# Optimization experiments

Measured on AMD Instinct MI355X. Metric: run time of the kernel, lower is better.

The kernel has to match this reference:

```python
import jax, jax.numpy as jnp
import numpy as np

SCALE = 0.08838834764831845  # 1/sqrt(head_size=128)
B, H, D, BS, NB, X, MAX_BLOCKS = 32, 16, 128, 16, 2048, 8, 64
S = MAX_BLOCKS * BS  # max context = 1024


def setup_inputs() -> dict:
    key = jax.random.key(0)
    ks = jax.random.split(key, 6)
    query = jax.random.normal(ks[0], (B, H, D), dtype=jnp.float32)
    new_k = jax.random.normal(ks[1], (B, H, D), dtype=jnp.float32)
    new_v = jax.random.normal(ks[2], (B, H, D), dtype=jnp.float32)
    # vLLM paged layouts: key [NB, H, D//X, BS, X], value [NB, H, BS, D]
    key_cache = jax.random.normal(ks[3], (NB, H, D // X, BS, X), dtype=jnp.float32)
    value_cache = jax.random.normal(ks[4], (NB, H, BS, D), dtype=jnp.float32)
    # non-overlapping block tables: seq i owns blocks [i*64, (i+1)*64)
    block_tables = jnp.arange(B * MAX_BLOCKS, dtype=jnp.int32).reshape(B, MAX_BLOCKS)
    context_lens = jax.random.randint(ks[5], (B,), 256, S + 1).astype(jnp.int32)
    last = context_lens - 1  # slot of the token being decoded
    slot_mapping = (block_tables[jnp.arange(B), last // BS] * BS + last % BS).astype(jnp.int32)
    return dict(query=query, key=new_k, value=new_v, key_cache=key_cache,
                value_cache=value_cache, block_tables=block_tables,
                context_lens=context_lens, slot_mapping=slot_mapping)


def reference(query, key, value, key_cache, value_cache, block_tables, context_lens, slot_mapping):
    nb, h, hsx, bs, x = key_cache.shape
    d = hsx * x
    # flatten paged caches to [nb*bs, h, d] slot-major views
    k_flat = jnp.transpose(key_cache, (0, 3, 1, 2, 4)).reshape(nb * bs, h, d)
    v_flat = jnp.transpose(value_cache, (0, 2, 1, 3)).reshape(nb * bs, h, d)
    # ops.reshape_and_cache: write the new token's k/v into its slot
    k_flat = k_flat.at[slot_mapping].set(key)
    v_flat = v_flat.at[slot_mapping].set(value)
    # single_query_cached_kv_attention, fully vectorized over tokens
    s = block_tables.shape[1] * bs
    pos = jnp.arange(s)
    tok = block_tables[:, pos // bs] * bs + pos % bs        # [B, S] flat slot ids
    keys = k_flat[tok]                                       # [B, S, H, D] gather
    vals = v_flat[tok]                                       # [B, S, H, D]
    scores = jnp.einsum('bhd,bshd->bhs', query, keys) * jnp.float32(SCALE)
    mask = pos[None, :] < context_lens[:, None]              # valid context positions
    scores = jnp.where(mask[:, None, :], scores, jnp.float32(-1e9))
    attn = jax.nn.softmax(scores, axis=-1)
    out = jnp.einsum('bhs,bshd->bhd', attn, vals)            # [B, H, D]
    return out.reshape(out.shape[0], h * d)
```

## Files before the change

### kernel.cpp

```cpp
#include <hip/hip_runtime.h>
#include <math.h>

#define BB 32
#define HH 16
#define DD 128
#define BSZ 16
#define MAXBLK 64
#define NCHUNK 4
#define CT 256
#define CBLK 16
#define SCALE 0.08838834764831845f

__global__ __launch_bounds__(256) void attn_chunk_kernel(
    const float* __restrict__ q, const float* __restrict__ newk,
    const float* __restrict__ newv, const float* __restrict__ kc,
    const float* __restrict__ vc, const int* __restrict__ block_tables,
    const int* __restrict__ context_lens,
    float* __restrict__ o_part, float* __restrict__ m_part,
    float* __restrict__ l_part)
{
    __shared__ __align__(16) float s_scores[CT];
    __shared__ __align__(16) float s_q[DD];
    __shared__ float s_red[8];
    __shared__ __align__(16) float s_out[4][DD];

    int gid  = blockIdx.x;
    int c    = gid & (NCHUNK - 1);
    int bh   = gid >> 2;
    int b    = bh >> 4;
    int h    = bh & 15;
    int tid  = threadIdx.x;
    int wave = tid >> 6;
    int lane = tid & 63;

    int len    = context_lens[b];
    int cstart = c * CT;
    if (cstart >= len) return;

    int nblk   = (len + 15) >> 4;
    int cb0    = c * CBLK;
    int cb_end = min(nblk, cb0 + CBLK);
    int last   = len - 1;
    bool haslast = (last >> 8) == c;

    if (tid < DD) s_q[tid] = q[(size_t)bh * DD + tid] * SCALE;
    __syncthreads();

    int hi = lane >> 5;
    int xq = lane & 1;
    int tk = (lane >> 1) & 15;

    float4 rq[8];
#pragma unroll
    for (int ch = 0; ch < 8; ++ch)
        rq[ch] = *(const float4*)&s_q[(2 * ch + hi) * 8 + 4 * xq];

    const int* bt = block_tables + b * MAXBLK;

    for (int cb = cb0 + wave; cb < cb_end; cb += 4) {
        int pb = bt[cb];
        const float* kbase = kc + ((size_t)pb * HH + h) * 2048 + 4 * lane;
        float acc = 0.f;
#pragma unroll
        for (int ch = 0; ch < 8; ++ch) {
            float4 kv = *(const float4*)(kbase + ch * 256);
            acc += rq[ch].x * kv.x + rq[ch].y * kv.y
                 + rq[ch].z * kv.z + rq[ch].w * kv.w;
        }
        acc += __shfl_xor(acc, 1);
        acc += __shfl_xor(acc, 32);
        if (lane < 32 && (lane & 1) == 0) {
            int p = cb * 16 + tk;
            s_scores[(cb - cb0) * 16 + tk] = (p < len) ? acc : -INFINITY;
        }
    }
    __syncthreads();

    if (haslast && wave == 0) {
        float2 nk = *(const float2*)&newk[(size_t)bh * DD + 2 * lane];
        float part = s_q[2 * lane] * nk.x + s_q[2 * lane + 1] * nk.y;
#pragma unroll
        for (int off = 32; off; off >>= 1) part += __shfl_xor(part, off);
        if (lane == 0) s_scores[last - cstart] = part;
    }
    __syncthreads();

    int padded = (cb_end - cb0) * 16;
    float mloc = (tid < padded) ? s_scores[tid] : -INFINITY;
#pragma unroll
    for (int off = 32; off; off >>= 1) mloc = fmaxf(mloc, __shfl_xor(mloc, off));
    if (lane == 0) s_red[wave] = mloc;
    __syncthreads();
    float m = fmaxf(fmaxf(s_red[0], s_red[1]), fmaxf(s_red[2], s_red[3]));

    float e = 0.f;
    if (tid < padded) {
        e = __expf(s_scores[tid] - m);
        s_scores[tid] = e;
    }
    float ssum = e;
#pragma unroll
    for (int off = 32; off; off >>= 1) ssum += __shfl_xor(ssum, off);
    if (lane == 0) s_red[4 + wave] = ssum;
    __syncthreads();
    float lsum = s_red[4] + s_red[5] + s_red[6] + s_red[7];

    int dv = 4 * (lane & 31);
    float4 nv4 = make_float4(0.f, 0.f, 0.f, 0.f);
    if (haslast) nv4 = *(const float4*)&newv[(size_t)bh * DD + dv];
    int lastTok = haslast ? last : -1;

    float4 acc4 = make_float4(0.f, 0.f, 0.f, 0.f);
    for (int cb = cb0 + wave; cb < cb_end; cb += 4) {
        int pb = bt[cb];
        const float* vbase = vc + ((size_t)pb * HH + h) * 2048 + 4 * lane;
        int base_s = (cb - cb0) * 16 + hi;
        int base_p = cb * 16 + hi;
#pragma unroll
        for (int t2 = 0; t2 < 8; ++t2) {
            float w = s_scores[base_s + 2 * t2];
            float4 vv = *(const float4*)(vbase + t2 * 256);
            if (base_p + 2 * t2 == lastTok) vv = nv4;
            acc4.x += w * vv.x;
            acc4.y += w * vv.y;
            acc4.z += w * vv.z;
            acc4.w += w * vv.w;
        }
    }
    acc4.x += __shfl_xor(acc4.x, 32);
    acc4.y += __shfl_xor(acc4.y, 32);
    acc4.z += __shfl_xor(acc4.z, 32);
    acc4.w += __shfl_xor(acc4.w, 32);
    if (lane < 32) *(float4*)&s_out[wave][dv] = acc4;
    __syncthreads();

    if (tid < DD) {
        float o = s_out[0][tid] + s_out[1][tid] + s_out[2][tid] + s_out[3][tid];
        o_part[(size_t)gid * DD + tid] = o;
    }
    if (tid == 0) {
        m_part[gid] = m;
        l_part[gid] = lsum;
    }
}

__global__ __launch_bounds__(128) void attn_combine_kernel(
    const float* __restrict__ o_part, const float* __restrict__ m_part,
    const float* __restrict__ l_part, const int* __restrict__ context_lens,
    float* __restrict__ out)
{
    int bh  = blockIdx.x;
    int b   = bh >> 4;
    int tid = threadIdx.x;
    int len = context_lens[b];
    int nc  = (len + CT - 1) >> 8;

    float mi[NCHUNK];
    float m_g = -INFINITY;
    for (int i = 0; i < nc; ++i) {
        mi[i] = m_part[bh * NCHUNK + i];
        m_g = fmaxf(m_g, mi[i]);
    }
    float acc = 0.f, lg = 0.f;
    for (int i = 0; i < nc; ++i) {
        float w = __expf(mi[i] - m_g);
        lg  += w * l_part[bh * NCHUNK + i];
        acc += w * o_part[(size_t)(bh * NCHUNK + i) * DD + tid];
    }
    out[(size_t)bh * DD + tid] = acc / lg;
}

extern "C" void kernel_launch(void* const* d_in, const int* in_sizes, int n_in,
                              void* d_out, int out_size, void* d_ws, size_t ws_size,
                              hipStream_t stream) {
    const float* query        = (const float*)d_in[0];
    const float* key          = (const float*)d_in[1];
    const float* value        = (const float*)d_in[2];
    const float* key_cache    = (const float*)d_in[3];
    const float* value_cache  = (const float*)d_in[4];
    const int*   block_tables = (const int*)d_in[5];
    const int*   context_lens = (const int*)d_in[6];
    float*       out          = (float*)d_out;

    float* o_part = (float*)d_ws;
    float* m_part = o_part + (size_t)BB * HH * NCHUNK * DD;
    float* l_part = m_part + (size_t)BB * HH * NCHUNK;

    attn_chunk_kernel<<<BB * HH * NCHUNK, 256, 0, stream>>>(
        query, key, value, key_cache, value_cache, block_tables,
        context_lens, o_part, m_part, l_part);
    attn_combine_kernel<<<BB * HH, 128, 0, stream>>>(
        o_part, m_part, l_part, context_lens, out);
}
```

Baseline: 492.0 us.

## Fuse QK and PV into a single-pass online softmax per wave

```diff
diff --git a/kernel.cpp b/kernel.cpp
--- a/kernel.cpp
+++ b/kernel.cpp
@@ -4,7 +4,6 @@
 #define BB 32
 #define HH 16
 #define DD 128
-#define BSZ 16
 #define MAXBLK 64
 #define NCHUNK 4
 #define CT 256
@@ -19,10 +18,10 @@
     float* __restrict__ o_part, float* __restrict__ m_part,
     float* __restrict__ l_part)
 {
-    __shared__ __align__(16) float s_scores[CT];
     __shared__ __align__(16) float s_q[DD];
-    __shared__ float s_red[8];
-    __shared__ __align__(16) float s_out[4][DD];
+    __shared__ __align__(16) float s_o[4][DD];
+    __shared__ float s_m[4];
+    __shared__ float s_l[4];
 
     int gid  = blockIdx.x;
     int c    = gid & (NCHUNK - 1);
@@ -49,98 +48,101 @@
     int hi = lane >> 5;
     int xq = lane & 1;
     int tk = (lane >> 1) & 15;
+    int dv = 4 * (lane & 31);
 
     float4 rq[8];
 #pragma unroll
     for (int ch = 0; ch < 8; ++ch)
         rq[ch] = *(const float4*)&s_q[(2 * ch + hi) * 8 + 4 * xq];
 
-    const int* bt = block_tables + b * MAXBLK;
-
-    for (int cb = cb0 + wave; cb < cb_end; cb += 4) {
-        int pb = bt[cb];
-        const float* kbase = kc + ((size_t)pb * HH + h) * 2048 + 4 * lane;
-        float acc = 0.f;
-#pragma unroll
-        for (int ch = 0; ch < 8; ++ch) {
-            float4 kv = *(const float4*)(kbase + ch * 256);
-            acc += rq[ch].x * kv.x + rq[ch].y * kv.y
-                 + rq[ch].z * kv.z + rq[ch].w * kv.w;
-        }
-        acc += __shfl_xor(acc, 1);
-        acc += __shfl_xor(acc, 32);
-        if (lane < 32 && (lane & 1) == 0) {
-            int p = cb * 16 + tk;
-            s_scores[(cb - cb0) * 16 + tk] = (p < len) ? acc : -INFINITY;
-        }
-    }
-    __syncthreads();
-
-    if (haslast && wave == 0) {
+    float s_last = 0.f;
+    float4 nv4 = make_float4(0.f, 0.f, 0.f, 0.f);
+    if (haslast) {
         float2 nk = *(const float2*)&newk[(size_t)bh * DD + 2 * lane];
         float part = s_q[2 * lane] * nk.x + s_q[2 * lane + 1] * nk.y;
 #pragma unroll
         for (int off = 32; off; off >>= 1) part += __shfl_xor(part, off);
-        if (lane == 0) s_scores[last - cstart] = part;
+        s_last = part;
+        nv4 = *(const float4*)&newv[(size_t)bh * DD + dv];
     }
-    __syncthreads();
-
-    int padded = (cb_end - cb0) * 16;
-    float mloc = (tid < padded) ? s_scores[tid] : -INFINITY;
-#pragma unroll
-    for (int off = 32; off; off >>= 1) mloc = fmaxf(mloc, __shfl_xor(mloc, off));
-    if (lane == 0) s_red[wave] = mloc;
-    __syncthreads();
-    float m = fmaxf(fmaxf(s_red[0], s_red[1]), fmaxf(s_red[2], s_red[3]));
-
-    float e = 0.f;
-    if (tid < padded) {
-        e = __expf(s_scores[tid] - m);
-        s_scores[tid] = e;
-    }
-    float ssum = e;
-#pragma unroll
-    for (int off = 32; off; off >>= 1) ssum += __shfl_xor(ssum, off);
-    if (lane == 0) s_red[4 + wave] = ssum;
-    __syncthreads();
-    float lsum = s_red[4] + s_red[5] + s_red[6] + s_red[7];
-
-    int dv = 4 * (lane & 31);
-    float4 nv4 = make_float4(0.f, 0.f, 0.f, 0.f);
-    if (haslast) nv4 = *(const float4*)&newv[(size_t)bh * DD + dv];
     int lastTok = haslast ? last : -1;
 
-    float4 acc4 = make_float4(0.f, 0.f, 0.f, 0.f);
+    const int* bt = block_tables + b * MAXBLK;
+
+    float  m_run = -INFINITY;
+    float  l_run = 0.f;
+    float4 acc4  = make_float4(0.f, 0.f, 0.f, 0.f);
+
+#pragma unroll 1
     for (int cb = cb0 + wave; cb < cb_end; cb += 4) {
         int pb = bt[cb];
+        const float* kbase = kc + ((size_t)pb * HH + h) * 2048 + 4 * lane;
         const float* vbase = vc + ((size_t)pb * HH + h) * 2048 + 4 * lane;
-        int base_s = (cb - cb0) * 16 + hi;
-        int base_p = cb * 16 + hi;
+
+        float4 kf[8], vf[8];
+#pragma unroll
+        for (int i = 0; i < 8; ++i) kf[i] = *(const float4*)(kbase + i * 256);
+#pragma unroll
+        for (int i = 0; i < 8; ++i) vf[i] = *(const float4*)(vbase + i * 256);
+
+        float sc = 0.f;
+#pragma unroll
+        for (int i = 0; i < 8; ++i)
+            sc += rq[i].x * kf[i].x + rq[i].y * kf[i].y
+                + rq[i].z * kf[i].z + rq[i].w * kf[i].w;
+        sc += __shfl_xor(sc, 1);
+        sc += __shfl_xor(sc, 32);
+        int p = cb * 16 + tk;
+        if (p == lastTok) sc = s_last;
+        if (p >= len)     sc = -INFINITY;
+
+        float bm = sc;
+        bm = fmaxf(bm, __shfl_xor(bm, 2));
+        bm = fmaxf(bm, __shfl_xor(bm, 4));
+        bm = fmaxf(bm, __shfl_xor(bm, 8));
+        bm = fmaxf(bm, __shfl_xor(bm, 16));
+
+        float mnew  = fmaxf(m_run, bm);
+        float scale = __expf(m_run - mnew);
+        acc4.x *= scale; acc4.y *= scale; acc4.z *= scale; acc4.w *= scale;
+
+        float lsum8 = 0.f;
 #pragma unroll
         for (int t2 = 0; t2 < 8; ++t2) {
-            float w = s_scores[base_s + 2 * t2];
-            float4 vv = *(const float4*)(vbase + t2 * 256);
-            if (base_p + 2 * t2 == lastTok) vv = nv4;
-            acc4.x += w * vv.x;
-            acc4.y += w * vv.y;
-            acc4.z += w * vv.z;
-            acc4.w += w * vv.w;
+            int tt = 2 * t2 + hi;
+            float st  = __shfl(sc, 4 * t2 + 2 * hi);
+            float wgt = __expf(st - mnew);
+            lsum8 += wgt;
+            float4 vv = vf[t2];
+            if (cb * 16 + tt == lastTok) vv = nv4;
+            acc4.x += wgt * vv.x;
+            acc4.y += wgt * vv.y;
+            acc4.z += wgt * vv.z;
+            acc4.w += wgt * vv.w;
         }
+        l_run = l_run * scale + lsum8 + __shfl_xor(lsum8, 32);
+        m_run = mnew;
     }
+
     acc4.x += __shfl_xor(acc4.x, 32);
     acc4.y += __shfl_xor(acc4.y, 32);
     acc4.z += __shfl_xor(acc4.z, 32);
     acc4.w += __shfl_xor(acc4.w, 32);
-    if (lane < 32) *(float4*)&s_out[wave][dv] = acc4;
+    if (lane < 32) *(float4*)&s_o[wave][dv] = acc4;
+    if (lane == 0) { s_m[wave] = m_run; s_l[wave] = l_run; }
     __syncthreads();
 
     if (tid < DD) {
-        float o = s_out[0][tid] + s_out[1][tid] + s_out[2][tid] + s_out[3][tid];
+        float mg = fmaxf(fmaxf(s_m[0], s_m[1]), fmaxf(s_m[2], s_m[3]));
+        float w0 = __expf(s_m[0] - mg), w1 = __expf(s_m[1] - mg);
+        float w2 = __expf(s_m[2] - mg), w3 = __expf(s_m[3] - mg);
+        float o = w0 * s_o[0][tid] + w1 * s_o[1][tid]
+                + w2 * s_o[2][tid] + w3 * s_o[3][tid];
         o_part[(size_t)gid * DD + tid] = o;
-    }
-    if (tid == 0) {
-        m_part[gid] = m;
-        l_part[gid] = lsum;
+        if (tid == 0) {
+            m_part[gid] = mg;
+            l_part[gid] = w0 * s_l[0] + w1 * s_l[1] + w2 * s_l[2] + w3 * s_l[3];
+        }
     }
 }
 
```

Measured after the change: 485.4 us. About the same (-1.4%).
